# Performance work log

Hardware: AMD Instinct MI355X
Metric: run time of the kernel (lower is better)

Reference implementation:

```python
import jax, jax.numpy as jnp
import numpy as np
from jax.ops import segment_sum

IN_DIM, HID_DIM, OUT_DIM = 128, 128, 64
N_NODES, N_EDGES = 50000, 800000


def gcn_conv(x, src, dst, W, b, n_nodes):
    # Symmetric GCN normalization (no self loops): deg at targets from unit weights
    deg = segment_sum(jnp.ones(src.shape[0], dtype=x.dtype), dst, num_segments=n_nodes)
    dinv = jnp.where(deg > 0, jax.lax.rsqrt(jnp.maximum(deg, 1.0)), 0.0)
    norm = dinv[src] * dinv[dst]                      # [E]
    h = x @ W                                         # [N, out] small GEMM first (PyG order)
    msg = h[src] * norm[:, None]                      # gather + scale: [E, out]
    out = segment_sum(msg, dst, num_segments=n_nodes) # scatter-add to targets
    return out + b


def setup_inputs() -> dict:
    key = jax.random.key(0)
    k1, k2, k3, k4, k5 = jax.random.split(key, 5)
    x = jax.random.normal(k1, (N_NODES, IN_DIM), dtype=jnp.float32)
    edge_index = jax.random.randint(k2, (2, N_EDGES), 0, N_NODES, dtype=jnp.int64)
    s1 = 1.0 / np.sqrt(IN_DIM)
    s2 = 1.0 / np.sqrt(HID_DIM)
    W1 = jax.random.uniform(k3, (IN_DIM, HID_DIM), jnp.float32, -s1, s1)
    b1 = jnp.zeros((HID_DIM,), jnp.float32)
    W2 = jax.random.uniform(k4, (HID_DIM, OUT_DIM), jnp.float32, -s2, s2)
    b2 = jnp.zeros((OUT_DIM,), jnp.float32)
    return {"x": x, "edge_index": edge_index, "W1": W1, "b1": b1, "W2": W2, "b2": b2}


def reference(x, edge_index, W1, b1, W2, b2):
    n_nodes = x.shape[0]
    src, dst = edge_index[0], edge_index[1]
    h = gcn_conv(x, src, dst, W1, b1, n_nodes)
    h = jax.nn.relu(h)
    # Dropout is identity in eval mode (reference is deterministic)
    out = gcn_conv(h, src, dst, W2, b2, n_nodes)
    return out
```

## Files before the change

kernel.cpp:

```cpp
#include <hip/hip_runtime.h>

#define N_NODES 50000
#define N_EDGES 800000
#define IN_DIM  128
#define HID_DIM 128
#define OUT_DIM 64

#define NPAD 50176
#define CAP  64
#define GEMM1B ((N_NODES + 63) / 64)
#define FILLB (N_EDGES / 256)
#define W2PREPB 8

typedef __attribute__((ext_vector_type(8))) short bf16x8;
typedef __attribute__((ext_vector_type(4))) float f32x4;
typedef __attribute__((ext_vector_type(2))) float f32x2;

__device__ __forceinline__ unsigned short f2bf(float f) {
    unsigned u = __float_as_uint(f);
    u += 0x7fffu + ((u >> 16) & 1u);
    return (unsigned short)(u >> 16);
}
__device__ __forceinline__ float bflo(unsigned u) { return __uint_as_float(u << 16); }
__device__ __forceinline__ float bfhi(unsigned u) { return __uint_as_float(u & 0xffff0000u); }

#define ACC8(u)  do { \
    acc[0] += bflo(u.x); acc[1] += bfhi(u.x); \
    acc[2] += bflo(u.y); acc[3] += bfhi(u.y); \
    acc[4] += bflo(u.z); acc[5] += bfhi(u.z); \
    acc[6] += bflo(u.w); acc[7] += bfhi(u.w); } while (0)

__device__ __forceinline__ unsigned char f2fp8(float f) {
    return (unsigned char)(__builtin_amdgcn_cvt_pk_fp8_f32(f, f, 0, false) & 0xff);
}

#define FMAF8(u, sc_)  do { \
    f32x2 p0 = __builtin_amdgcn_cvt_pk_f32_fp8((int)u.x, false); \
    f32x2 p1 = __builtin_amdgcn_cvt_pk_f32_fp8((int)u.x, true);  \
    f32x2 p2 = __builtin_amdgcn_cvt_pk_f32_fp8((int)u.y, false); \
    f32x2 p3 = __builtin_amdgcn_cvt_pk_f32_fp8((int)u.y, true);  \
    acc[0] += p0[0] * (sc_); acc[1] += p0[1] * (sc_); \
    acc[2] += p1[0] * (sc_); acc[3] += p1[1] * (sc_); \
    acc[4] += p2[0] * (sc_); acc[5] += p2[1] * (sc_); \
    acc[6] += p3[0] * (sc_); acc[7] += p3[1] * (sc_); } while (0)

__device__ __forceinline__ float deg2dinv(int deg) {
    return (deg > 0) ? rsqrtf((float)deg) : 0.0f;
}

#define W1T_STRIDE 136


__global__ __launch_bounds__(256) void gemm1_kernel(const float* __restrict__ x,
                                                    const float* __restrict__ W1,
                                                    int* __restrict__ cnt,
                                                    unsigned char* __restrict__ h1f8) {
    __shared__ unsigned short w1t[128 * W1T_STRIDE];

    int tid = threadIdx.x;
    int zi = blockIdx.x * 256 + tid;
    if (zi < NPAD / 4) {
        int4 z = {0, 0, 0, 0};
        ((int4*)cnt)[zi] = z;
    }

#pragma unroll
    for (int i = 0; i < 64; ++i) {
        int idx = i * 256 + tid;
        int k = idx >> 7, c = idx & 127;
        w1t[c * W1T_STRIDE + k] = f2bf(W1[idx]);
    }
    __syncthreads();

    int wave = tid >> 6;
    int lane = tid & 63;
    int n = lane & 15, quad = lane >> 4;
    int row0 = blockIdx.x * 64 + wave * 16;

    int arow = row0 + n;
    if (arow >= N_NODES) arow = N_NODES - 1;
    const float* aptr = x + (size_t)arow * 128 + quad * 8;
    const unsigned short* bbase = w1t + (size_t)n * W1T_STRIDE + quad * 8;

    f32x4 acc[8];
#pragma unroll
    for (int t = 0; t < 8; ++t) acc[t] = (f32x4){0.f, 0.f, 0.f, 0.f};

#pragma unroll
    for (int w4 = 0; w4 < 4; ++w4) {
        float4 f0 = *(const float4*)(aptr + w4 * 32);
        float4 f1 = *(const float4*)(aptr + w4 * 32 + 4);
        bf16x8 af;
        af[0] = (short)f2bf(f0.x); af[1] = (short)f2bf(f0.y);
        af[2] = (short)f2bf(f0.z); af[3] = (short)f2bf(f0.w);
        af[4] = (short)f2bf(f1.x); af[5] = (short)f2bf(f1.y);
        af[6] = (short)f2bf(f1.z); af[7] = (short)f2bf(f1.w);
#pragma unroll
        for (int t = 0; t < 8; ++t) {
            bf16x8 bf = *(const bf16x8*)(bbase + (size_t)t * 16 * W1T_STRIDE + w4 * 32);
            acc[t] = __builtin_amdgcn_mfma_f32_16x16x32_bf16(af, bf, acc[t], 0, 0, 0);
        }
    }

#pragma unroll
    for (int r = 0; r < 4; ++r) {
        int row = row0 + quad * 4 + r;
        if (row < N_NODES) {
            unsigned char* o = h1f8 + (size_t)row * 128 + n;
#pragma unroll
            for (int t = 0; t < 8; ++t) o[t * 16] = f2fp8(acc[t][r]);
        }
    }
}


__global__ __launch_bounds__(256) void prep_fill_kernel(const int* __restrict__ src,
                                                        const int* __restrict__ dst,
                                                        int* __restrict__ cnt,
                                                        unsigned short* __restrict__ csr_src,
                                                        const float* __restrict__ W2,
                                                        unsigned short* __restrict__ w2t) {
    int bid = blockIdx.x;
    int tid = threadIdx.x;
    if (bid < W2PREPB) {
        int idx = bid * 256 + tid;
        int c = idx >> 5, k4 = (idx & 31) * 4;
        ushort4 o;
        o.x = f2bf(W2[(k4 + 0) * 64 + c]);
        o.y = f2bf(W2[(k4 + 1) * 64 + c]);
        o.z = f2bf(W2[(k4 + 2) * 64 + c]);
        o.w = f2bf(W2[(k4 + 3) * 64 + c]);
        *(ushort4*)(w2t + c * 128 + k4) = o;
    } else {
        int e = (bid - W2PREPB) * 256 + tid;
        int s = src[e], d = dst[e];
        int slot = atomicAdd(&cnt[d], 1);
        if (slot < CAP) csr_src[(d << 6) + slot] = (unsigned short)s;
    }
}


#define A1T_STRIDE 136

__global__ __launch_bounds__(256) void agg1_gemm2_fused(const unsigned short* __restrict__ csr_src,
                                                        const int* __restrict__ cnt,
                                                        const float* __restrict__ b1,
                                                        const unsigned char* __restrict__ h1f8,
                                                        const unsigned short* __restrict__ w2t,
                                                        unsigned short* __restrict__ h2b) {
    __shared__ unsigned short a1t[16 * A1T_STRIDE];

    int node0 = blockIdx.x * 16;
    int g = threadIdx.x >> 4;
    int q = threadIdx.x & 15;
    int node = node0 + g;
    int start = node << 6;
    int m = cnt[node];
    float dn = deg2dinv(m);
    if (m > CAP) m = CAP;

    float acc[8] = {};
    int j = 0;
    for (; j + 7 < m; j += 8) {
        ushort4 sa = *(const ushort4*)(csr_src + start + j);
        ushort4 sb = *(const ushort4*)(csr_src + start + j + 4);
        float d0 = deg2dinv(cnt[sa.x]);
        float d1 = deg2dinv(cnt[sa.y]);
        float d2 = deg2dinv(cnt[sa.z]);
        float d3 = deg2dinv(cnt[sa.w]);
        float d4 = deg2dinv(cnt[sb.x]);
        float d5 = deg2dinv(cnt[sb.y]);
        float d6 = deg2dinv(cnt[sb.z]);
        float d7 = deg2dinv(cnt[sb.w]);
        uint2 u0 = ((const uint2*)(h1f8 + (size_t)sa.x * 128))[q];
        uint2 u1 = ((const uint2*)(h1f8 + (size_t)sa.y * 128))[q];
        uint2 u2 = ((const uint2*)(h1f8 + (size_t)sa.z * 128))[q];
        uint2 u3 = ((const uint2*)(h1f8 + (size_t)sa.w * 128))[q];
        uint2 u4 = ((const uint2*)(h1f8 + (size_t)sb.x * 128))[q];
        uint2 u5 = ((const uint2*)(h1f8 + (size_t)sb.y * 128))[q];
        uint2 u6 = ((const uint2*)(h1f8 + (size_t)sb.z * 128))[q];
        uint2 u7 = ((const uint2*)(h1f8 + (size_t)sb.w * 128))[q];
        FMAF8(u0, d0); FMAF8(u1, d1); FMAF8(u2, d2); FMAF8(u3, d3);
        FMAF8(u4, d4); FMAF8(u5, d5); FMAF8(u6, d6); FMAF8(u7, d7);
    }
    for (; j + 3 < m; j += 4) {
        ushort4 sa = *(const ushort4*)(csr_src + start + j);
        float d0 = deg2dinv(cnt[sa.x]);
        float d1 = deg2dinv(cnt[sa.y]);
        float d2 = deg2dinv(cnt[sa.z]);
        float d3 = deg2dinv(cnt[sa.w]);
        uint2 u0 = ((const uint2*)(h1f8 + (size_t)sa.x * 128))[q];
        uint2 u1 = ((const uint2*)(h1f8 + (size_t)sa.y * 128))[q];
        uint2 u2 = ((const uint2*)(h1f8 + (size_t)sa.z * 128))[q];
        uint2 u3 = ((const uint2*)(h1f8 + (size_t)sa.w * 128))[q];
        FMAF8(u0, d0); FMAF8(u1, d1); FMAF8(u2, d2); FMAF8(u3, d3);
    }
    for (; j < m; ++j) {
        int s0 = csr_src[start + j];
        float d0 = deg2dinv(cnt[s0]);
        uint2 u0 = ((const uint2*)(h1f8 + (size_t)s0 * 128))[q];
        FMAF8(u0, d0);
    }

    {
        float4 bA = ((const float4*)b1)[2 * q];
        float4 bB = ((const float4*)b1)[2 * q + 1];
        ushort4 oA, oB;
        oA.x = f2bf(fmaxf(acc[0] * dn + bA.x, 0.f));
        oA.y = f2bf(fmaxf(acc[1] * dn + bA.y, 0.f));
        oA.z = f2bf(fmaxf(acc[2] * dn + bA.z, 0.f));
        oA.w = f2bf(fmaxf(acc[3] * dn + bA.w, 0.f));
        oB.x = f2bf(fmaxf(acc[4] * dn + bB.x, 0.f));
        oB.y = f2bf(fmaxf(acc[5] * dn + bB.y, 0.f));
        oB.z = f2bf(fmaxf(acc[6] * dn + bB.z, 0.f));
        oB.w = f2bf(fmaxf(acc[7] * dn + bB.w, 0.f));
        ushort4* o = (ushort4*)(a1t + g * A1T_STRIDE + q * 8);
        o[0] = oA;
        o[1] = oB;
    }
    __syncthreads();

    int wave = threadIdx.x >> 6;
    int lane = threadIdx.x & 63;
    int n = lane & 15, quad = lane >> 4;
    const unsigned short* bbase = w2t + (size_t)(wave * 16 + n) * 128 + quad * 8;
    const unsigned short* abase = a1t + (size_t)n * A1T_STRIDE + quad * 8;

    f32x4 c2 = (f32x4){0.f, 0.f, 0.f, 0.f};
#pragma unroll
    for (int w4 = 0; w4 < 4; ++w4) {
        bf16x8 af = *(const bf16x8*)(abase + w4 * 32);
        bf16x8 bf = *(const bf16x8*)(bbase + w4 * 32);
        c2 = __builtin_amdgcn_mfma_f32_16x16x32_bf16(af, bf, c2, 0, 0, 0);
    }

#pragma unroll
    for (int r = 0; r < 4; ++r) {
        int row = node0 + quad * 4 + r;
        float dr = deg2dinv(cnt[row]);
        h2b[(size_t)row * 64 + wave * 16 + n] = f2bf(c2[r] * dr);
    }
}


__global__ __launch_bounds__(256) void agg2_kernel(const unsigned short* __restrict__ csr_src,
                                                   const int* __restrict__ cnt,
                                                   const float* __restrict__ b2,
                                                   const unsigned short* __restrict__ h2b,
                                                   float* __restrict__ out) {
    int node = blockIdx.x * 4 + (threadIdx.x >> 6);
    if (node >= N_NODES) return;
    int lane = threadIdx.x & 63;
    int grp = lane >> 3;
    int q   = lane & 7;
    int start = node << 6;
    int m = cnt[node];
    float dn = deg2dinv(m);
    if (m > CAP) m = CAP;

    float acc[8] = {};

    int j = grp;
    for (; j + 8 < m; j += 16) {
        int s0 = csr_src[start + j];
        int s1 = csr_src[start + j + 8];
        uint4 u0 = ((const uint4*)(h2b + (size_t)s0 * 64))[q];
        uint4 u1 = ((const uint4*)(h2b + (size_t)s1 * 64))[q];
        ACC8(u0); ACC8(u1);
    }
    if (j < m) {
        int s0 = csr_src[start + j];
        uint4 u0 = ((const uint4*)(h2b + (size_t)s0 * 64))[q];
        ACC8(u0);
    }

#pragma unroll
    for (int d = 8; d <= 32; d <<= 1) {
#pragma unroll
        for (int c = 0; c < 8; ++c) acc[c] += __shfl_xor(acc[c], d, 64);
    }

    if (lane < 8) {
        float4 bA = ((const float4*)b2)[2 * q];
        float4 bB = ((const float4*)b2)[2 * q + 1];
        float4 rA, rB;
        rA.x = acc[0] * dn + bA.x;
        rA.y = acc[1] * dn + bA.y;
        rA.z = acc[2] * dn + bA.z;
        rA.w = acc[3] * dn + bA.w;
        rB.x = acc[4] * dn + bB.x;
        rB.y = acc[5] * dn + bB.y;
        rB.z = acc[6] * dn + bB.z;
        rB.w = acc[7] * dn + bB.w;
        float4* o = (float4*)(out + (size_t)node * 64);
        o[2 * q] = rA;
        o[2 * q + 1] = rB;
    }
}


extern "C" void kernel_launch(void* const* d_in, const int* in_sizes, int n_in,
                              void* d_out, int out_size, void* d_ws, size_t ws_size,
                              hipStream_t stream) {
    const float* x  = (const float*)d_in[0];
    const int*   ei = (const int*)d_in[1];
    const float* W1 = (const float*)d_in[2];
    const float* b1 = (const float*)d_in[3];
    const float* W2 = (const float*)d_in[4];
    const float* b2 = (const float*)d_in[5];
    float* out = (float*)d_out;

    const int* src = ei;
    const int* dst = ei + N_EDGES;

    char* ws = (char*)d_ws;
    int*   cnt       = (int*)ws;
    unsigned short* csr_src = (unsigned short*)(cnt + NPAD);
    unsigned char* h1f8 = (unsigned char*)(csr_src + (size_t)N_NODES * CAP);
    unsigned short* h2b = (unsigned short*)(h1f8 + (size_t)N_NODES * HID_DIM);
    unsigned short* w2t = h2b + (size_t)N_NODES * OUT_DIM;

    gemm1_kernel<<<GEMM1B, 256, 0, stream>>>(x, W1, cnt, h1f8);

    prep_fill_kernel<<<W2PREPB + FILLB, 256, 0, stream>>>(src, dst, cnt, csr_src,
                                                          W2, w2t);

    agg1_gemm2_fused<<<N_NODES / 16, 256, 0, stream>>>(csr_src, cnt, b1, h1f8, w2t, h2b);

    agg2_kernel<<<(N_NODES + 3) / 4, 256, 0, stream>>>(csr_src, cnt, b2, h2b, out);
}
```

Baseline: 184.2 us.

## Fold source-side degree normalization into GEMM1 epilogue before fp8 quantization

```diff
diff --git a/kernel.cpp b/kernel.cpp
--- a/kernel.cpp
+++ b/kernel.cpp
@@ -34,84 +34,21 @@
     return (unsigned char)(__builtin_amdgcn_cvt_pk_fp8_f32(f, f, 0, false) & 0xff);
 }
 
-#define FMAF8(u, sc_)  do { \
+#define ACCF8(u)  do { \
     f32x2 p0 = __builtin_amdgcn_cvt_pk_f32_fp8((int)u.x, false); \
     f32x2 p1 = __builtin_amdgcn_cvt_pk_f32_fp8((int)u.x, true);  \
     f32x2 p2 = __builtin_amdgcn_cvt_pk_f32_fp8((int)u.y, false); \
     f32x2 p3 = __builtin_amdgcn_cvt_pk_f32_fp8((int)u.y, true);  \
-    acc[0] += p0[0] * (sc_); acc[1] += p0[1] * (sc_); \
-    acc[2] += p1[0] * (sc_); acc[3] += p1[1] * (sc_); \
-    acc[4] += p2[0] * (sc_); acc[5] += p2[1] * (sc_); \
-    acc[6] += p3[0] * (sc_); acc[7] += p3[1] * (sc_); } while (0)
+    acc[0] += p0[0]; acc[1] += p0[1]; \
+    acc[2] += p1[0]; acc[3] += p1[1]; \
+    acc[4] += p2[0]; acc[5] += p2[1]; \
+    acc[6] += p3[0]; acc[7] += p3[1]; } while (0)
 
 __device__ __forceinline__ float deg2dinv(int deg) {
     return (deg > 0) ? rsqrtf((float)deg) : 0.0f;
 }
 
 #define W1T_STRIDE 136
-
-
-__global__ __launch_bounds__(256) void gemm1_kernel(const float* __restrict__ x,
-                                                    const float* __restrict__ W1,
-                                                    int* __restrict__ cnt,
-                                                    unsigned char* __restrict__ h1f8) {
-    __shared__ unsigned short w1t[128 * W1T_STRIDE];
-
-    int tid = threadIdx.x;
-    int zi = blockIdx.x * 256 + tid;
-    if (zi < NPAD / 4) {
-        int4 z = {0, 0, 0, 0};
-        ((int4*)cnt)[zi] = z;
-    }
-
-#pragma unroll
-    for (int i = 0; i < 64; ++i) {
-        int idx = i * 256 + tid;
-        int k = idx >> 7, c = idx & 127;
-        w1t[c * W1T_STRIDE + k] = f2bf(W1[idx]);
-    }
-    __syncthreads();
-
-    int wave = tid >> 6;
-    int lane = tid & 63;
-    int n = lane & 15, quad = lane >> 4;
-    int row0 = blockIdx.x * 64 + wave * 16;
-
-    int arow = row0 + n;
-    if (arow >= N_NODES) arow = N_NODES - 1;
-    const float* aptr = x + (size_t)arow * 128 + quad * 8;
-    const unsigned short* bbase = w1t + (size_t)n * W1T_STRIDE + quad * 8;
-
-    f32x4 acc[8];
-#pragma unroll
-    for (int t = 0; t < 8; ++t) acc[t] = (f32x4){0.f, 0.f, 0.f, 0.f};
-
-#pragma unroll
-    for (int w4 = 0; w4 < 4; ++w4) {
-        float4 f0 = *(const float4*)(aptr + w4 * 32);
-        float4 f1 = *(const float4*)(aptr + w4 * 32 + 4);
-        bf16x8 af;
-        af[0] = (short)f2bf(f0.x); af[1] = (short)f2bf(f0.y);
-        af[2] = (short)f2bf(f0.z); af[3] = (short)f2bf(f0.w);
-        af[4] = (short)f2bf(f1.x); af[5] = (short)f2bf(f1.y);
-        af[6] = (short)f2bf(f1.z); af[7] = (short)f2bf(f1.w);
-#pragma unroll
-        for (int t = 0; t < 8; ++t) {
-            bf16x8 bf = *(const bf16x8*)(bbase + (size_t)t * 16 * W1T_STRIDE + w4 * 32);
-            acc[t] = __builtin_amdgcn_mfma_f32_16x16x32_bf16(af, bf, acc[t], 0, 0, 0);
-        }
-    }
-
-#pragma unroll
-    for (int r = 0; r < 4; ++r) {
-        int row = row0 + quad * 4 + r;
-        if (row < N_NODES) {
-            unsigned char* o = h1f8 + (size_t)row * 128 + n;
-#pragma unroll
-            for (int t = 0; t < 8; ++t) o[t * 16] = f2fp8(acc[t][r]);
-        }
-    }
-}
 
 
 __global__ __launch_bounds__(256) void prep_fill_kernel(const int* __restrict__ src,
@@ -140,6 +77,64 @@
 }
 
 
+__global__ __launch_bounds__(256) void gemm1_kernel(const float* __restrict__ x,
+                                                    const float* __restrict__ W1,
+                                                    const int* __restrict__ cnt,
+                                                    unsigned char* __restrict__ h1f8) {
+    __shared__ unsigned short w1t[128 * W1T_STRIDE];
+
+    int tid = threadIdx.x;
+#pragma unroll
+    for (int i = 0; i < 64; ++i) {
+        int idx = i * 256 + tid;
+        int k = idx >> 7, c = idx & 127;
+        w1t[c * W1T_STRIDE + k] = f2bf(W1[idx]);
+    }
+    __syncthreads();
+
+    int wave = tid >> 6;
+    int lane = tid & 63;
+    int n = lane & 15, quad = lane >> 4;
+    int row0 = blockIdx.x * 64 + wave * 16;
+
+    int arow = row0 + n;
+    if (arow >= N_NODES) arow = N_NODES - 1;
+    const float* aptr = x + (size_t)arow * 128 + quad * 8;
+    const unsigned short* bbase = w1t + (size_t)n * W1T_STRIDE + quad * 8;
+
+    f32x4 acc[8];
+#pragma unroll
+    for (int t = 0; t < 8; ++t) acc[t] = (f32x4){0.f, 0.f, 0.f, 0.f};
+
+#pragma unroll
+    for (int w4 = 0; w4 < 4; ++w4) {
+        float4 f0 = *(const float4*)(aptr + w4 * 32);
+        float4 f1 = *(const float4*)(aptr + w4 * 32 + 4);
+        bf16x8 af;
+        af[0] = (short)f2bf(f0.x); af[1] = (short)f2bf(f0.y);
+        af[2] = (short)f2bf(f0.z); af[3] = (short)f2bf(f0.w);
+        af[4] = (short)f2bf(f1.x); af[5] = (short)f2bf(f1.y);
+        af[6] = (short)f2bf(f1.z); af[7] = (short)f2bf(f1.w);
+#pragma unroll
+        for (int t = 0; t < 8; ++t) {
+            bf16x8 bf = *(const bf16x8*)(bbase + (size_t)t * 16 * W1T_STRIDE + w4 * 32);
+            acc[t] = __builtin_amdgcn_mfma_f32_16x16x32_bf16(af, bf, acc[t], 0, 0, 0);
+        }
+    }
+
+#pragma unroll
+    for (int r = 0; r < 4; ++r) {
+        int row = row0 + quad * 4 + r;
+        if (row < N_NODES) {
+            float dn = deg2dinv(cnt[row]);
+            unsigned char* o = h1f8 + (size_t)row * 128 + n;
+#pragma unroll
+            for (int t = 0; t < 8; ++t) o[t * 16] = f2fp8(acc[t][r] * dn);
+        }
+    }
+}
+
+
 #define A1T_STRIDE 136
 
 __global__ __launch_bounds__(256) void agg1_gemm2_fused(const unsigned short* __restrict__ csr_src,
@@ -164,14 +159,6 @@
     for (; j + 7 < m; j += 8) {
         ushort4 sa = *(const ushort4*)(csr_src + start + j);
         ushort4 sb = *(const ushort4*)(csr_src + start + j + 4);
-        float d0 = deg2dinv(cnt[sa.x]);
-        float d1 = deg2dinv(cnt[sa.y]);
-        float d2 = deg2dinv(cnt[sa.z]);
-        float d3 = deg2dinv(cnt[sa.w]);
-        float d4 = deg2dinv(cnt[sb.x]);
-        float d5 = deg2dinv(cnt[sb.y]);
-        float d6 = deg2dinv(cnt[sb.z]);
-        float d7 = deg2dinv(cnt[sb.w]);
         uint2 u0 = ((const uint2*)(h1f8 + (size_t)sa.x * 128))[q];
         uint2 u1 = ((const uint2*)(h1f8 + (size_t)sa.y * 128))[q];
         uint2 u2 = ((const uint2*)(h1f8 + (size_t)sa.z * 128))[q];
@@ -180,26 +167,21 @@
         uint2 u5 = ((const uint2*)(h1f8 + (size_t)sb.y * 128))[q];
         uint2 u6 = ((const uint2*)(h1f8 + (size_t)sb.z * 128))[q];
         uint2 u7 = ((const uint2*)(h1f8 + (size_t)sb.w * 128))[q];
-        FMAF8(u0, d0); FMAF8(u1, d1); FMAF8(u2, d2); FMAF8(u3, d3);
-        FMAF8(u4, d4); FMAF8(u5, d5); FMAF8(u6, d6); FMAF8(u7, d7);
+        ACCF8(u0); ACCF8(u1); ACCF8(u2); ACCF8(u3);
+        ACCF8(u4); ACCF8(u5); ACCF8(u6); ACCF8(u7);
     }
     for (; j + 3 < m; j += 4) {
         ushort4 sa = *(const ushort4*)(csr_src + start + j);
-        float d0 = deg2dinv(cnt[sa.x]);
-        float d1 = deg2dinv(cnt[sa.y]);
-        float d2 = deg2dinv(cnt[sa.z]);
-        float d3 = deg2dinv(cnt[sa.w]);
         uint2 u0 = ((const uint2*)(h1f8 + (size_t)sa.x * 128))[q];
         uint2 u1 = ((const uint2*)(h1f8 + (size_t)sa.y * 128))[q];
         uint2 u2 = ((const uint2*)(h1f8 + (size_t)sa.z * 128))[q];
         uint2 u3 = ((const uint2*)(h1f8 + (size_t)sa.w * 128))[q];
-        FMAF8(u0, d0); FMAF8(u1, d1); FMAF8(u2, d2); FMAF8(u3, d3);
+        ACCF8(u0); ACCF8(u1); ACCF8(u2); ACCF8(u3);
     }
     for (; j < m; ++j) {
         int s0 = csr_src[start + j];
-        float d0 = deg2dinv(cnt[s0]);
         uint2 u0 = ((const uint2*)(h1f8 + (size_t)s0 * 128))[q];
-        FMAF8(u0, d0);
+        ACCF8(u0);
     }
 
     {
@@ -320,11 +302,13 @@
     unsigned short* h2b = (unsigned short*)(h1f8 + (size_t)N_NODES * HID_DIM);
     unsigned short* w2t = h2b + (size_t)N_NODES * OUT_DIM;
 
-    gemm1_kernel<<<GEMM1B, 256, 0, stream>>>(x, W1, cnt, h1f8);
+    (void)hipMemsetAsync(cnt, 0, NPAD * sizeof(int), stream);
 
     prep_fill_kernel<<<W2PREPB + FILLB, 256, 0, stream>>>(src, dst, cnt, csr_src,
                                                           W2, w2t);
 
+    gemm1_kernel<<<GEMM1B, 256, 0, stream>>>(x, W1, cnt, h1f8);
+
     agg1_gemm2_fused<<<N_NODES / 16, 256, 0, stream>>>(csr_src, cnt, b1, h1f8, w2t, h2b);
 
     agg2_kernel<<<(N_NODES + 3) / 4, 256, 0, stream>>>(csr_src, cnt, b2, h2b, out);
```

Result: faster. 179.6 us, median of 2 (-2.5%).
